# Optimization experiments

Hardware: AMD Instinct MI355X
Metric: run time of the kernel (lower is better)

## Reference

```python
import jax, jax.numpy as jnp
import numpy as np
from jax import lax

B, N_BASES, C_IN, C_OUT, K, HW = 32, 5, 128, 128, 3, 56

def setup_inputs() -> dict:
    key = jax.random.key(0)
    k1, k2, k3 = jax.random.split(key, 3)
    x = jax.random.normal(k1, (B, C_IN, HW, HW), dtype=jnp.float32)
    weights = jax.random.normal(k2, (N_BASES, C_OUT, C_IN, K, K), dtype=jnp.float32) * 0.05
    scales = jax.random.uniform(k3, (N_BASES,), dtype=jnp.float32)
    return {"x": x, "weights": weights, "scales": scales}

def _binarize(w):
    # per-base: sign(w) * mean(|w|) over the whole weight tensor of that base
    m = jnp.mean(jnp.abs(w), axis=(1, 2, 3, 4), keepdims=True)  # [N,1,1,1,1]
    return jnp.sign(w) * m

def reference(x, weights, scales):
    # torch pads with constant value 1 (not zero) once, then all bases share it
    xp = jnp.pad(x, ((0, 0), (0, 0), (1, 1), (1, 1)), constant_values=1.0)
    wq = _binarize(weights)                              # [N,O,I,K,K]
    wf = wq.reshape(N_BASES * C_OUT, C_IN, K, K)          # fuse bases into one conv
    out = lax.conv_general_dilated(
        xp, wf, window_strides=(1, 1), padding='VALID',
        dimension_numbers=('NCHW', 'OIHW', 'NCHW'))      # [B, N*O, H, W]
    out = out.reshape(B, N_BASES, C_OUT, HW, HW)
    return jnp.einsum('bnohw,n->bohw', out, scales)
```

## Files before the change

### kernel.cpp

```cpp
#include <hip/hip_runtime.h>
#include <stdint.h>

#define N_BASES 5
#define WELEM (128 * 128 * 3 * 3)

typedef __attribute__((ext_vector_type(4))) float f32x4;
typedef __attribute__((ext_vector_type(8))) short bf16x8;
typedef __attribute__((ext_vector_type(4))) unsigned short u16x4;

__device__ __forceinline__ unsigned short f2bf(float v) {
  union { float f; uint32_t u; } un;
  un.f = v;
  uint32_t r = un.u + 0x7FFFu + ((un.u >> 16) & 1u);
  return (unsigned short)(r >> 16);
}

__global__ __launch_bounds__(256) void prep_fused(
    const float* __restrict__ x, const float* __restrict__ w,
    unsigned short* __restrict__ xp, float* __restrict__ csum_part) {
  int bi = blockIdx.x;
  if (bi >= 1856) {
    int id = bi - 1856;
    int n = id >> 6;
    int chunk = id & 63;
    const f32x4* wb = (const f32x4*)(w + (size_t)n * WELEM + chunk * 2304);
    float s = 0.f;
    for (int i = threadIdx.x; i < 576; i += 256) {
      f32x4 v = wb[i];
      s += fabsf(v.x) + fabsf(v.y) + fabsf(v.z) + fabsf(v.w);
    }
    #pragma unroll
    for (int off = 32; off > 0; off >>= 1) s += __shfl_down(s, off);
    __shared__ float red[4];
    if ((threadIdx.x & 63) == 0) red[threadIdx.x >> 6] = s;
    __syncthreads();
    if (threadIdx.x == 0) csum_part[id] = red[0] + red[1] + red[2] + red[3];
    return;
  }
  int tid = threadIdx.x;
  int b = bi / 58;
  int hp = bi - b * 58;
  unsigned short* dst = xp + ((size_t)b * 58 + hp) * 58 * 128;
  int gh = hp - 1;
  uint4 ones = make_uint4(0x3F803F80u, 0x3F803F80u, 0x3F803F80u, 0x3F803F80u);
  if ((unsigned)gh >= 56u) {
    for (int i = tid; i < 928; i += 256) ((uint4*)dst)[i] = ones;
    return;
  }
  __shared__ unsigned short tile[56 * 128];
  const float* xb = x + (size_t)b * 128 * 3136 + (size_t)gh * 56;
  #pragma unroll
  for (int k = 0; k < 7; ++k) {
    int g = k * 256 + tid;
    int c4 = g / 56;
    int ww = g - c4 * 56;
    const float* sp = xb + (size_t)(4 * c4) * 3136 + ww;
    u16x4 pk;
    pk.x = f2bf(sp[0]);
    pk.y = f2bf(sp[3136]);
    pk.z = f2bf(sp[2 * 3136]);
    pk.w = f2bf(sp[3 * 3136]);
    *(u16x4*)&tile[ww * 128 + ((c4 ^ ((ww & 15) << 1)) << 2)] = pk;
  }
  __syncthreads();
  for (int i = tid; i < 928; i += 256) {
    int wp = i >> 4;
    int e = i & 15;
    uint4 v;
    if (wp == 0 || wp == 57) {
      v = ones;
    } else {
      int r = wp - 1;
      v = *(const uint4*)&tile[r * 128 + (((2 * e) ^ ((r & 15) << 1)) << 2)];
    }
    *(uint4*)(dst + (size_t)wp * 128 + e * 8) = v;
  }
}

__global__ __launch_bounds__(256) void binweight_kernel(
    const float* __restrict__ w, const float* __restrict__ csum_part,
    const float* __restrict__ scales, unsigned short* __restrict__ wq) {
  __shared__ float parts[320];
  __shared__ float coef[N_BASES];
  for (int i = threadIdx.x; i < 320; i += 256) parts[i] = csum_part[i];
  __syncthreads();
  if (threadIdx.x < N_BASES) {
    float s = 0.f;
    #pragma unroll 8
    for (int k = 0; k < 64; ++k) s += parts[threadIdx.x * 64 + k];
    coef[threadIdx.x] = scales[threadIdx.x] * s * (1.0f / (float)WELEM);
  }
  __syncthreads();
  int f = blockIdx.x * 256 + threadIdx.x;
  float s = 0.f;
  #pragma unroll
  for (int n = 0; n < N_BASES; ++n) {
    float cn = coef[n];
    float v = w[n * WELEM + f];
    s += (v > 0.f) ? cn : ((v < 0.f) ? -cn : 0.f);
  }
  int o = f / 1152;
  int rem = f - o * 1152;
  int i = rem / 9;
  int t = rem - i * 9;
  int kb = i >> 5;
  int quad = (i >> 3) & 3;
  int e = i & 7;
  wq[((size_t)((t * 4 + kb) * 4 + quad) * 128 + o) * 8 + e] = f2bf(s);
}

__global__ __launch_bounds__(256, 3) void conv_kernel(
    const unsigned short* __restrict__ xp, const unsigned short* __restrict__ wq,
    float* __restrict__ out) {
  __shared__ unsigned short patch[23040];

  const int tid = threadIdx.x;
  const int blk = blockIdx.x;
  const int b = blk & 31;
  const int tile = blk >> 5;
  const int hi = tile >> 2;
  const int wi = tile & 3;
  const int h0 = hi * 8;
  const int w0 = (wi == 3) ? 40 : wi * 16;

  const int lane = tid & 63;
  const int wave = tid >> 6;
  const int mh = wave >> 1;
  const int nh = wave & 1;
  const int l15 = lane & 15;
  const int quad = lane >> 4;

  const unsigned short* wlane =
      wq + ((size_t)quad * 128 + nh * 64 + l15) * 8;

  bf16x8 b0[4], b1[4], b2[4], b3[4];
  #pragma unroll
  for (int nf = 0; nf < 4; ++nf)
    b0[nf] = *(const bf16x8*)(wlane + nf * 128);
  #pragma unroll
  for (int nf = 0; nf < 4; ++nf)
    b1[nf] = *(const bf16x8*)(wlane + (size_t)4096 + nf * 128);

  const size_t rowstride = 58 * 128;
  for (int i = tid; i < 2880; i += 256) {
    int sp = i >> 4;
    int c16 = i & 15;
    int ph = sp / 18;
    int pw = sp - ph * 18;
    const unsigned short* gp = xp + ((size_t)b * 58 + (h0 + ph)) * rowstride +
                               (size_t)(w0 + pw) * 128 + c16 * 8;
    uint4 v = *(const uint4*)gp;
    *(uint4*)&patch[sp * 128 + ((c16 ^ (sp & 7)) << 3)] = v;
  }
  __syncthreads();

  f32x4 acc[4][4];
  #pragma unroll
  for (int mf = 0; mf < 4; ++mf)
    #pragma unroll
    for (int nf = 0; nf < 4; ++nf) acc[mf][nf] = (f32x4)0.f;

  auto pf_af = [&](int s, bf16x8 (&af)[4]) {
    const int sc = (s < 36) ? s : 35;
    const int t = sc >> 2;
    const int kb = sc & 3;
    const int kh = (t * 11) >> 5;
    const int kw = t - 3 * kh;
    #pragma unroll
    for (int mf = 0; mf < 4; ++mf) {
      const int sp = (mh * 4 + mf + kh) * 18 + l15 + kw;
      af[mf] = *(const bf16x8*)&patch[sp * 128 +
                                      (((kb * 4 + quad) ^ (sp & 7)) << 3)];
    }
  };
  auto pf_b = [&](int s, bf16x8 (&br)[4]) {
    const int sc = (s < 36) ? s : 35;
    #pragma unroll
    for (int nf = 0; nf < 4; ++nf)
      br[nf] = *(const bf16x8*)(wlane + (size_t)sc * 4096 + nf * 128);
  };
  auto compute = [&](bf16x8 (&af)[4], bf16x8 (&br)[4]) {
    #pragma unroll
    for (int mf = 0; mf < 4; ++mf)
      #pragma unroll
      for (int nf = 0; nf < 4; ++nf)
        acc[mf][nf] = __builtin_amdgcn_mfma_f32_16x16x32_bf16(
            af[mf], br[nf], acc[mf][nf], 0, 0, 0);
  };

  bf16x8 afA[4], afB[4];
  pf_af(0, afA);

  #pragma unroll 1
  for (int d = 0; d < 9; ++d) {
    const int s = d * 4;
    pf_af(s + 1, afB); pf_b(s + 2, b2); compute(afA, b0);
    pf_af(s + 2, afA); pf_b(s + 3, b3); compute(afB, b1);
    pf_af(s + 3, afB); pf_b(s + 4, b0); compute(afA, b2);
    pf_af(s + 4, afA); pf_b(s + 5, b1); compute(afB, b3);
  }

  #pragma unroll
  for (int mf = 0; mf < 4; ++mf) {
    int h = h0 + mh * 4 + mf;
    #pragma unroll
    for (int nf = 0; nf < 4; ++nf) {
      int o = nh * 64 + nf * 16 + l15;
      float* p = out + (((size_t)b * 128 + o) * 56 + h) * 56 + w0 + quad * 4;
      *(f32x4*)p = acc[mf][nf];
    }
  }
}

extern "C" void kernel_launch(void* const* d_in, const int* in_sizes, int n_in,
                              void* d_out, int out_size, void* d_ws, size_t ws_size,
                              hipStream_t stream) {
  const float* x = (const float*)d_in[0];
  const float* w = (const float*)d_in[1];
  const float* scales = (const float*)d_in[2];
  float* out = (float*)d_out;

  float* csum_part = (float*)d_ws;
  unsigned short* wq = (unsigned short*)((char*)d_ws + 4096);
  unsigned short* xpad = (unsigned short*)((char*)d_ws + 512 * 1024);

  prep_fused<<<1856 + 320, 256, 0, stream>>>(x, w, xpad, csum_part);
  binweight_kernel<<<576, 256, 0, stream>>>(w, csum_part, scales, wq);
  conv_kernel<<<28 * 32, 256, 0, stream>>>(xpad, wq, out);
}
```

Baseline: 146.0 us.

## Fuse input padding and bf16 conversion into conv kernel patch load

Drops the separate pass that padded x with ones and wrote a channel-last bf16 copy to the workspace. The conv kernel now reads fp32 NCHW x directly, converts each value to bf16, and fills out-of-bounds positions with 1.0 while staging its patch into shared memory. This removes one full write and re-read of the padded activation tensor. In exchange the patch loads become strided 4-byte gathers across channels, and halo pixels are re-read by neighbouring tiles, which may hurt load efficiency inside the conv kernel.

```diff
diff --git a/kernel.cpp b/kernel.cpp
--- a/kernel.cpp
+++ b/kernel.cpp
@@ -6,7 +6,6 @@
 
 typedef __attribute__((ext_vector_type(4))) float f32x4;
 typedef __attribute__((ext_vector_type(8))) short bf16x8;
-typedef __attribute__((ext_vector_type(4))) unsigned short u16x4;
 
 __device__ __forceinline__ unsigned short f2bf(float v) {
   union { float f; uint32_t u; } un;
@@ -15,66 +14,23 @@
   return (unsigned short)(r >> 16);
 }
 
-__global__ __launch_bounds__(256) void prep_fused(
-    const float* __restrict__ x, const float* __restrict__ w,
-    unsigned short* __restrict__ xp, float* __restrict__ csum_part) {
-  int bi = blockIdx.x;
-  if (bi >= 1856) {
-    int id = bi - 1856;
-    int n = id >> 6;
-    int chunk = id & 63;
-    const f32x4* wb = (const f32x4*)(w + (size_t)n * WELEM + chunk * 2304);
-    float s = 0.f;
-    for (int i = threadIdx.x; i < 576; i += 256) {
-      f32x4 v = wb[i];
-      s += fabsf(v.x) + fabsf(v.y) + fabsf(v.z) + fabsf(v.w);
-    }
-    #pragma unroll
-    for (int off = 32; off > 0; off >>= 1) s += __shfl_down(s, off);
-    __shared__ float red[4];
-    if ((threadIdx.x & 63) == 0) red[threadIdx.x >> 6] = s;
-    __syncthreads();
-    if (threadIdx.x == 0) csum_part[id] = red[0] + red[1] + red[2] + red[3];
-    return;
+__global__ __launch_bounds__(256) void wsum_kernel(
+    const float* __restrict__ w, float* __restrict__ csum_part) {
+  int id = blockIdx.x;
+  int n = id >> 6;
+  int chunk = id & 63;
+  const f32x4* wb = (const f32x4*)(w + (size_t)n * WELEM + chunk * 2304);
+  float s = 0.f;
+  for (int i = threadIdx.x; i < 576; i += 256) {
+    f32x4 v = wb[i];
+    s += fabsf(v.x) + fabsf(v.y) + fabsf(v.z) + fabsf(v.w);
   }
-  int tid = threadIdx.x;
-  int b = bi / 58;
-  int hp = bi - b * 58;
-  unsigned short* dst = xp + ((size_t)b * 58 + hp) * 58 * 128;
-  int gh = hp - 1;
-  uint4 ones = make_uint4(0x3F803F80u, 0x3F803F80u, 0x3F803F80u, 0x3F803F80u);
-  if ((unsigned)gh >= 56u) {
-    for (int i = tid; i < 928; i += 256) ((uint4*)dst)[i] = ones;
-    return;
-  }
-  __shared__ unsigned short tile[56 * 128];
-  const float* xb = x + (size_t)b * 128 * 3136 + (size_t)gh * 56;
   #pragma unroll
-  for (int k = 0; k < 7; ++k) {
-    int g = k * 256 + tid;
-    int c4 = g / 56;
-    int ww = g - c4 * 56;
-    const float* sp = xb + (size_t)(4 * c4) * 3136 + ww;
-    u16x4 pk;
-    pk.x = f2bf(sp[0]);
-    pk.y = f2bf(sp[3136]);
-    pk.z = f2bf(sp[2 * 3136]);
-    pk.w = f2bf(sp[3 * 3136]);
-    *(u16x4*)&tile[ww * 128 + ((c4 ^ ((ww & 15) << 1)) << 2)] = pk;
-  }
+  for (int off = 32; off > 0; off >>= 1) s += __shfl_down(s, off);
+  __shared__ float red[4];
+  if ((threadIdx.x & 63) == 0) red[threadIdx.x >> 6] = s;
   __syncthreads();
-  for (int i = tid; i < 928; i += 256) {
-    int wp = i >> 4;
-    int e = i & 15;
-    uint4 v;
-    if (wp == 0 || wp == 57) {
-      v = ones;
-    } else {
-      int r = wp - 1;
-      v = *(const uint4*)&tile[r * 128 + (((2 * e) ^ ((r & 15) << 1)) << 2)];
-    }
-    *(uint4*)(dst + (size_t)wp * 128 + e * 8) = v;
-  }
+  if (threadIdx.x == 0) csum_part[id] = red[0] + red[1] + red[2] + red[3];
 }
 
 __global__ __launch_bounds__(256) void binweight_kernel(
@@ -110,7 +66,7 @@
 }
 
 __global__ __launch_bounds__(256, 3) void conv_kernel(
-    const unsigned short* __restrict__ xp, const unsigned short* __restrict__ wq,
+    const float* __restrict__ x, const unsigned short* __restrict__ wq,
     float* __restrict__ out) {
   __shared__ unsigned short patch[23040];
 
@@ -141,16 +97,24 @@
   for (int nf = 0; nf < 4; ++nf)
     b1[nf] = *(const bf16x8*)(wlane + (size_t)4096 + nf * 128);
 
-  const size_t rowstride = 58 * 128;
+  const float* xb = x + (size_t)b * 128 * 3136;
   for (int i = tid; i < 2880; i += 256) {
     int sp = i >> 4;
     int c16 = i & 15;
     int ph = sp / 18;
     int pw = sp - ph * 18;
-    const unsigned short* gp = xp + ((size_t)b * 58 + (h0 + ph)) * rowstride +
-                               (size_t)(w0 + pw) * 128 + c16 * 8;
-    uint4 v = *(const uint4*)gp;
-    *(uint4*)&patch[sp * 128 + ((c16 ^ (sp & 7)) << 3)] = v;
+    int gh = h0 + ph - 1;
+    int gw = w0 + pw - 1;
+    union { uint4 q; unsigned short h[8]; } u;
+    if ((unsigned)gh < 56u && (unsigned)gw < 56u) {
+      const float* src = xb + (size_t)(c16 * 8) * 3136 + gh * 56 + gw;
+      #pragma unroll
+      for (int j = 0; j < 8; ++j) u.h[j] = f2bf(src[(size_t)j * 3136]);
+    } else {
+      #pragma unroll
+      for (int j = 0; j < 8; ++j) u.h[j] = 0x3F80;
+    }
+    *(uint4*)&patch[sp * 128 + ((c16 ^ (sp & 7)) << 3)] = u.q;
   }
   __syncthreads();
 
@@ -222,9 +186,8 @@
 
   float* csum_part = (float*)d_ws;
   unsigned short* wq = (unsigned short*)((char*)d_ws + 4096);
-  unsigned short* xpad = (unsigned short*)((char*)d_ws + 512 * 1024);
 
-  prep_fused<<<1856 + 320, 256, 0, stream>>>(x, w, xpad, csum_part);
+  wsum_kernel<<<320, 256, 0, stream>>>(w, csum_part);
   binweight_kernel<<<576, 256, 0, stream>>>(w, csum_part, scales, wq);
-  conv_kernel<<<28 * 32, 256, 0, stream>>>(xpad, wq, out);
+  conv_kernel<<<28 * 32, 256, 0, stream>>>(x, wq, out);
 }
```

Result: slower. 169.9 us (+16.4%).
